# Performance work log

Measured on AMD Instinct MI355X. Metric: run time of the kernel, lower is better.

Reference implementation:

```python
import jax, jax.numpy as jnp
import numpy as np

D_MODEL = 1024
NUM_HEADS = 16
HEAD_DIM = D_MODEL // NUM_HEADS
SCALE = HEAD_DIM ** -0.5
B, N = 4, 2048


def setup_inputs() -> dict:
    key = jax.random.key(0)
    ks = jax.random.split(key, 6)
    x = jax.random.normal(ks[0], (B, N, D_MODEL), dtype=jnp.float32)
    mask = jnp.ones((B, 1, N, N), dtype=jnp.int32)
    alibi_bias = jax.random.normal(ks[1], (1, NUM_HEADS, N, N), dtype=jnp.float32)
    s = 1.0 / np.sqrt(D_MODEL)
    Wq = jax.random.normal(ks[2], (D_MODEL, D_MODEL), dtype=jnp.float32) * s
    Wk = jax.random.normal(ks[3], (D_MODEL, D_MODEL), dtype=jnp.float32) * s
    Wv = jax.random.normal(ks[4], (D_MODEL, D_MODEL), dtype=jnp.float32) * s
    Wo = jax.random.normal(ks[5], (D_MODEL, D_MODEL), dtype=jnp.float32) * s
    return {"x": x, "mask": mask, "alibi_bias": alibi_bias,
            "Wq": Wq, "Wk": Wk, "Wv": Wv, "Wo": Wo}


def reference(x, mask, alibi_bias, Wq, Wk, Wv, Wo):
    Bx, Nx, D = x.shape
    H, Hd = NUM_HEADS, HEAD_DIM
    # torch Linear(bias=False): y = x @ W.T
    q = (x @ Wq.T).reshape(Bx, Nx, H, Hd).transpose(0, 2, 1, 3)  # [B,H,N,Hd]
    k = (x @ Wk.T).reshape(Bx, Nx, H, Hd).transpose(0, 2, 1, 3)
    v = (x @ Wv.T).reshape(Bx, Nx, H, Hd).transpose(0, 2, 1, 3)
    attn = jnp.einsum('bhqd,bhkd->bhqk', q, k) * SCALE
    attn = attn + alibi_bias
    neg_inf = jnp.finfo(attn.dtype).min
    attn = jnp.where(mask == 0, neg_inf, attn)
    attn = jax.nn.softmax(attn, axis=-1)
    out = jnp.einsum('bhqk,bhkd->bhqd', attn, v)  # [B,H,N,Hd]
    out = out.transpose(0, 2, 1, 3).reshape(Bx, Nx, D)
    return out @ Wo.T
```

## Files before the change

### kernel.cpp

```cpp
#include <hip/hip_runtime.h>

#define NSEQ 2048
#define DMODEL 1024
#define NHEAD 16
#define HDIM 64
#define NBATCH 4
#define MTOT 8192
#define ATT_SCALE 0.125f
#define LOG2E 1.4426950408889634f
#define SM_SHIFT 12.0f

typedef __bf16 bf16x8 __attribute__((ext_vector_type(8)));
typedef float f32x4 __attribute__((ext_vector_type(4)));
typedef unsigned int u32x4 __attribute__((ext_vector_type(4)));
typedef unsigned short u16;
typedef unsigned int u32;
typedef unsigned long long u64;

__device__ __forceinline__ u16 f2bf(float f) {
  u32 u = __builtin_bit_cast(u32, f);
  return (u16)((u + 0x7fffu + ((u >> 16) & 1u)) >> 16);
}

__device__ __forceinline__ void gload_lds16(const void* g, void* l) {
  __builtin_amdgcn_global_load_lds(
      (__attribute__((address_space(1))) const u32*)g,
      (__attribute__((address_space(3))) u32*)l, 16, 0, 0);
}

__global__ __launch_bounds__(256) void cast_f32_bf16(const float* __restrict__ in,
                                                     u16* __restrict__ out, int n) {
  int i = (blockIdx.x * 256 + threadIdx.x) * 4;
  if (i >= n) return;
  float4 v = *(const float4*)(in + i);
  ushort4 o;
  o.x = f2bf(v.x); o.y = f2bf(v.y); o.z = f2bf(v.z); o.w = f2bf(v.w);
  *(ushort4*)(out + i) = o;
}

__global__ __launch_bounds__(256) void cast_w4(const float* __restrict__ a,
                                               const float* __restrict__ b,
                                               const float* __restrict__ c,
                                               const float* __restrict__ d,
                                               u16* __restrict__ out) {
  int bid = blockIdx.x;
  int which = bid >> 10, lb = bid & 1023;
  const float* src = (which == 0) ? a : (which == 1) ? b : (which == 2) ? c : d;
  int i = (lb * 256 + threadIdx.x) * 4;
  float4 v = *(const float4*)(src + i);
  ushort4 o;
  o.x = f2bf(v.x); o.y = f2bf(v.y); o.z = f2bf(v.z); o.w = f2bf(v.w);
  *(ushort4*)(out + (size_t)which * 1048576 + i) = o;
}

__global__ __launch_bounds__(256) void pack_mask(const int* __restrict__ mask,
                                                 u64* __restrict__ bits) {
  int wave = (blockIdx.x * 256 + threadIdx.x) >> 6;
  int lane = threadIdx.x & 63;
  const int* row = mask + (size_t)wave * NSEQ;
  u64* out = bits + (size_t)wave * 32;
  for (int c = 0; c < 32; ++c) {
    int v = row[c * 64 + lane];
    u64 bl = __ballot(v != 0);
    if (lane == 0) out[c] = bl;
  }
}

__global__ __launch_bounds__(256) void gemm_qkv(const u16* __restrict__ A,
                                                const u16* __restrict__ Wc,
                                                u16* __restrict__ qo,
                                                u16* __restrict__ ko,
                                                u16* __restrict__ vo) {
  __shared__ __align__(16) u16 Al[128 * 64];
  __shared__ __align__(16) u16 Bl[128 * 64];
  const int tid = threadIdx.x;
  const int w = tid >> 6, l = tid & 63;
  const int l15 = l & 15, l4 = l >> 4;
  const int bm = blockIdx.x, bn = blockIdx.y;
  const int wm = w >> 1, wn = w & 1;

  f32x4 acc[4][4] = {};

  for (int ks = 0; ks < 1024; ks += 64) {
    __syncthreads();
#pragma unroll
    for (int c = 0; c < 4; ++c) {
      int g = w * 256 + c * 64 + l;
      int row = g >> 3, gc = g & 7;
      int sgc = gc ^ (row & 7);
      gload_lds16(A + (size_t)(bm * 128 + row) * 1024 + ks + sgc * 8, &Al[g * 8]);
      gload_lds16(Wc + (size_t)(bn * 128 + row) * 1024 + ks + sgc * 8, &Bl[g * 8]);
    }
    __syncthreads();
#pragma unroll
    for (int kc = 0; kc < 2; ++kc) {
      bf16x8 af[4], bfr[4];
#pragma unroll
      for (int mi = 0; mi < 4; ++mi) {
        int row = wm * 64 + mi * 16 + l15;
        int gc2 = (kc * 4 + l4) ^ (row & 7);
        af[mi] = *(const bf16x8*)&Al[row * 64 + gc2 * 8];
      }
#pragma unroll
      for (int ni = 0; ni < 4; ++ni) {
        int row = wn * 64 + ni * 16 + l15;
        int gc2 = (kc * 4 + l4) ^ (row & 7);
        bfr[ni] = *(const bf16x8*)&Bl[row * 64 + gc2 * 8];
      }
#pragma unroll
      for (int mi = 0; mi < 4; ++mi)
#pragma unroll
        for (int ni = 0; ni < 4; ++ni)
          acc[mi][ni] = __builtin_amdgcn_mfma_f32_16x16x32_bf16(af[mi], bfr[ni],
                                                                acc[mi][ni], 0, 0, 0);
    }
  }

  const int which = bn >> 3;
#pragma unroll
  for (int mi = 0; mi < 4; ++mi)
#pragma unroll
    for (int ni = 0; ni < 4; ++ni)
#pragma unroll
      for (int r = 0; r < 4; ++r) {
        int m = bm * 128 + wm * 64 + mi * 16 + l4 * 4 + r;
        int n = (bn & 7) * 128 + wn * 64 + ni * 16 + l15;
        int b = m >> 11, row = m & 2047, h = n >> 6, d = n & 63;
        u16 val = f2bf(acc[mi][ni][r]);
        size_t bh = (size_t)(b * 16 + h);
        if (which == 0)      qo[(bh * NSEQ + row) * 64 + d] = val;
        else if (which == 1) ko[(bh * NSEQ + row) * 64 + d] = val;
        else                 vo[(bh * 64 + d) * NSEQ + row] = val;
      }
}

__global__ __launch_bounds__(256) void gemm_out(const u16* __restrict__ A,
                                                const u16* __restrict__ W,
                                                float* __restrict__ C) {
  __shared__ __align__(16) u16 Al[128 * 64];
  __shared__ __align__(16) u16 Bl[128 * 64];
  const int tid = threadIdx.x;
  const int w = tid >> 6, l = tid & 63;
  const int l15 = l & 15, l4 = l >> 4;
  const int bm = blockIdx.x, bn = blockIdx.y;
  const int wm = w >> 1, wn = w & 1;

  f32x4 acc[4][4] = {};

  for (int ks = 0; ks < 1024; ks += 64) {
    __syncthreads();
#pragma unroll
    for (int c = 0; c < 4; ++c) {
      int g = w * 256 + c * 64 + l;
      int row = g >> 3, gc = g & 7;
      int sgc = gc ^ (row & 7);
      gload_lds16(A + (size_t)(bm * 128 + row) * 1024 + ks + sgc * 8, &Al[g * 8]);
      gload_lds16(W + (size_t)(bn * 128 + row) * 1024 + ks + sgc * 8, &Bl[g * 8]);
    }
    __syncthreads();
#pragma unroll
    for (int kc = 0; kc < 2; ++kc) {
      bf16x8 af[4], bfr[4];
#pragma unroll
      for (int mi = 0; mi < 4; ++mi) {
        int row = wm * 64 + mi * 16 + l15;
        int gc2 = (kc * 4 + l4) ^ (row & 7);
        af[mi] = *(const bf16x8*)&Al[row * 64 + gc2 * 8];
      }
#pragma unroll
      for (int ni = 0; ni < 4; ++ni) {
        int row = wn * 64 + ni * 16 + l15;
        int gc2 = (kc * 4 + l4) ^ (row & 7);
        bfr[ni] = *(const bf16x8*)&Bl[row * 64 + gc2 * 8];
      }
#pragma unroll
      for (int mi = 0; mi < 4; ++mi)
#pragma unroll
        for (int ni = 0; ni < 4; ++ni)
          acc[mi][ni] = __builtin_amdgcn_mfma_f32_16x16x32_bf16(af[mi], bfr[ni],
                                                                acc[mi][ni], 0, 0, 0);
    }
  }

#pragma unroll
  for (int mi = 0; mi < 4; ++mi)
#pragma unroll
    for (int ni = 0; ni < 4; ++ni)
#pragma unroll
      for (int r = 0; r < 4; ++r) {
        int m = bm * 128 + wm * 64 + mi * 16 + l4 * 4 + r;
        int n = bn * 128 + wn * 64 + ni * 16 + l15;
        C[(size_t)m * 1024 + n] = acc[mi][ni][r];
      }
}

__global__ __launch_bounds__(256, 4) void attn_kernel(
    const u16* __restrict__ q, const u16* __restrict__ k, const u16* __restrict__ vT,
    const float* __restrict__ alibi, const u64* __restrict__ mbits,
    u16* __restrict__ o) {
  __shared__ __align__(16) u16 Kl[2][64 * 64];
  __shared__ __align__(16) u16 Vl[2][64 * 64];

  const int tid = threadIdx.x, w = tid >> 6, l = tid & 63;
  const int l15 = l & 15, l4 = l >> 4;
  const int W = blockIdx.x;
  const int W2 = (W & 7) * 256 + (W >> 3);
  const int b = W2 & 3, hq = W2 >> 2;
  const int qb = hq & 31, h = hq >> 5;
  const int bh = b * 16 + h;
  const int wq0 = qb * 64 + w * 16;
  const int myq = wq0 + l15;

  bf16x8 aq[2];
  {
    const u16* qrow = q + ((size_t)bh * NSEQ + myq) * 64;
    aq[0] = *(const bf16x8*)(qrow + l4 * 8);
    aq[1] = *(const bf16x8*)(qrow + 32 + l4 * 8);
  }

  const u16* kg[2]; const u16* vg[2];
#pragma unroll
  for (int c = 0; c < 2; ++c) {
    int g = w * 128 + c * 64 + l;
    int row = g >> 3, gc = g & 7, sgc = gc ^ (row & 7);
    int srow = (row & 0x23) | (((row >> 2) & 3) << 3) | (((row >> 4) & 1) << 2);
    kg[c] = k + ((size_t)bh * NSEQ + srow) * 64 + sgc * 8;
    vg[c] = vT + ((size_t)bh * 64 + row) * NSEQ + sgc * 8;
  }

  const float* alp = alibi + (size_t)h * NSEQ * NSEQ + (size_t)myq * NSEQ + 8 * l4;
  const u64* mrp = mbits + ((size_t)b * NSEQ + myq) * 32;

  const int kfr[2] = { l15 * 128 + (((0 + l4) ^ (l15 & 7)) << 4),
                       l15 * 128 + (((4 + l4) ^ (l15 & 7)) << 4) };

  const u32x4 onesu = {0x3F803F80u, 0x3F803F80u, 0x3F803F80u, 0x3F803F80u};
  const bf16x8 bones = __builtin_bit_cast(bf16x8, onesu);

  f32x4 oacc[4] = {};
  f32x4 osum = {};

  auto stage = [&](u16* KB, u16* VB) {
#pragma unroll
    for (int c = 0; c < 2; ++c) {
      gload_lds16(kg[c], (char*)KB + (w * 128 + c * 64 + l) * 16);
      kg[c] += 4096;
      gload_lds16(vg[c], (char*)VB + (w * 128 + c * 64 + l) * 16);
      vg[c] += 64;
    }
  };

  auto loadal = [&](float4* a, u64& m, int t) {
    a[0] = *(const float4*)(alp + t * 64);
    a[1] = *(const float4*)(alp + t * 64 + 4);
    a[2] = *(const float4*)(alp + t * 64 + 32);
    a[3] = *(const float4*)(alp + t * 64 + 36);
    m = mrp[t];
  };

  float4 alA[4], alB[4];
  u64 mbA, mbB;

  stage(Kl[0], Vl[0]);
  loadal(alA, mbA, 0);
  __syncthreads();

  auto body = [&](const u16* KB, const u16* VB, u16* KN, u16* VN,
                  const float4* alc, u64 mbc, float4* aln, u64& mbn,
                  int t, bool dost) {
    if (dost) {
      loadal(aln, mbn, t + 1);
      stage(KN, VN);
    }

    f32x4 st[4];
#pragma unroll
    for (int kb = 0; kb < 4; ++kb) {
      f32x4 z = {0.f, 0.f, 0.f, 0.f};
      st[kb] = z;
#pragma unroll
      for (int kc = 0; kc < 2; ++kc) {
        bf16x8 bk = *(const bf16x8*)((const char*)KB + kfr[kc] + kb * 2048);
        st[kb] = __builtin_amdgcn_mfma_f32_16x16x32_bf16(bk, aq[kc], st[kb], 0, 0, 0);
      }
    }

#pragma unroll
    for (int kb = 0; kb < 4; ++kb)
#pragma unroll
      for (int r = 0; r < 4; ++r)
        st[kb][r] = fmaf(st[kb][r], ATT_SCALE, alc[kb][r]);
    if (!__all(mbc == ~0ull)) {
#pragma unroll
      for (int kb = 0; kb < 4; ++kb)
#pragma unroll
        for (int r = 0; r < 4; ++r) {
          int bit = 32 * (kb >> 1) + 8 * l4 + 4 * (kb & 1) + r;
          if (!((mbc >> bit) & 1)) st[kb][r] = -3.0e38f;
        }
    }

    float p[16];
#pragma unroll
    for (int kb = 0; kb < 4; ++kb)
#pragma unroll
      for (int r = 0; r < 4; ++r)
        p[kb * 4 + r] = exp2f(fmaf(st[kb][r], LOG2E, -SM_SHIFT * LOG2E));

    u32 Wp[8];
#pragma unroll
    for (int i = 0; i < 8; ++i)
      asm("v_cvt_pk_bf16_f32 %0, %1, %2" : "=v"(Wp[i]) : "v"(p[2 * i]), "v"(p[2 * i + 1]));

#pragma unroll
    for (int c = 0; c < 2; ++c) {
      u32x4 wv = {Wp[4 * c], Wp[4 * c + 1], Wp[4 * c + 2], Wp[4 * c + 3]};
      bf16x8 pa = __builtin_bit_cast(bf16x8, wv);
      osum = __builtin_amdgcn_mfma_f32_16x16x32_bf16(pa, bones, osum, 0, 0, 0);
#pragma unroll
      for (int db = 0; db < 4; ++db) {
        bf16x8 bv = *(const bf16x8*)((const char*)VB + kfr[c] + db * 2048);
        oacc[db] = __builtin_amdgcn_mfma_f32_16x16x32_bf16(pa, bv, oacc[db], 0, 0, 0);
      }
    }
    __syncthreads();
  };

  for (int t2 = 0; t2 < 16; ++t2) {
    body(Kl[0], Vl[0], Kl[1], Vl[1], alA, mbA, alB, mbB, t2 * 2, true);
    body(Kl[1], Vl[1], Kl[0], Vl[0], alB, mbB, alA, mbA, t2 * 2 + 1, t2 < 15);
  }

#pragma unroll
  for (int r = 0; r < 4; ++r) {
    float inv = __builtin_amdgcn_rcpf(osum[r]);
    int qq = wq0 + l4 * 4 + r;
#pragma unroll
    for (int db = 0; db < 4; ++db) {
      int d = db * 16 + l15;
      o[((size_t)b * NSEQ + qq) * DMODEL + h * 64 + d] = f2bf(oacc[db][r] * inv);
    }
  }
}

extern "C" void kernel_launch(void* const* d_in, const int* in_sizes, int n_in,
                              void* d_out, int out_size, void* d_ws, size_t ws_size,
                              hipStream_t stream) {
  (void)in_sizes; (void)n_in; (void)out_size; (void)ws_size;
  const float* x = (const float*)d_in[0];
  const int* mask = (const int*)d_in[1];
  const float* alibi = (const float*)d_in[2];
  const float* Wq = (const float*)d_in[3];
  const float* Wk = (const float*)d_in[4];
  const float* Wv = (const float*)d_in[5];
  const float* Wo = (const float*)d_in[6];
  float* out = (float*)d_out;

  char* ws = (char*)d_ws;
  const size_t MB = 1u << 20;
  u16* xb  = (u16*)(ws + 0 * MB);
  u16* wqb = (u16*)(ws + 16 * MB);
  u16* wob = (u16*)(ws + 22 * MB);
  u16* qb  = (u16*)(ws + 24 * MB);
  u16* kb  = (u16*)(ws + 40 * MB);
  u16* vT  = (u16*)(ws + 56 * MB);
  u16* ob  = (u16*)(ws + 72 * MB);
  u64* mbits = (u64*)(ws + 88 * MB);

  cast_f32_bf16<<<8192, 256, 0, stream>>>(x, xb, MTOT * DMODEL);
  cast_w4<<<4096, 256, 0, stream>>>(Wq, Wk, Wv, Wo, wqb);
  pack_mask<<<2048, 256, 0, stream>>>(mask, mbits);

  gemm_qkv<<<dim3(64, 24), 256, 0, stream>>>(xb, wqb, qb, kb, vT);

  attn_kernel<<<2048, 256, 0, stream>>>(qb, kb, vT, alibi, mbits, ob);

  gemm_out<<<dim3(64, 8), 256, 0, stream>>>(ob, wob, out);
}
```

Baseline: 412.7 us.

## Load attention K/V fragments directly into registers, dropping LDS staging

New measurement: 755.7 us. 1.83x slower.

```diff
diff --git a/kernel.cpp b/kernel.cpp
--- a/kernel.cpp
+++ b/kernel.cpp
@@ -194,13 +194,10 @@
       }
 }
 
-__global__ __launch_bounds__(256, 4) void attn_kernel(
+__global__ __launch_bounds__(256, 3) void attn_kernel(
     const u16* __restrict__ q, const u16* __restrict__ k, const u16* __restrict__ vT,
     const float* __restrict__ alibi, const u64* __restrict__ mbits,
     u16* __restrict__ o) {
-  __shared__ __align__(16) u16 Kl[2][64 * 64];
-  __shared__ __align__(16) u16 Vl[2][64 * 64];
-
   const int tid = threadIdx.x, w = tid >> 6, l = tid & 63;
   const int l15 = l & 15, l4 = l >> 4;
   const int W = blockIdx.x;
@@ -211,126 +208,105 @@
   const int wq0 = qb * 64 + w * 16;
   const int myq = wq0 + l15;
 
-  bf16x8 aq[2];
+  bf16x8 aq0, aq1;
   {
     const u16* qrow = q + ((size_t)bh * NSEQ + myq) * 64;
-    aq[0] = *(const bf16x8*)(qrow + l4 * 8);
-    aq[1] = *(const bf16x8*)(qrow + 32 + l4 * 8);
-  }
-
-  const u16* kg[2]; const u16* vg[2];
-#pragma unroll
-  for (int c = 0; c < 2; ++c) {
-    int g = w * 128 + c * 64 + l;
-    int row = g >> 3, gc = g & 7, sgc = gc ^ (row & 7);
-    int srow = (row & 0x23) | (((row >> 2) & 3) << 3) | (((row >> 4) & 1) << 2);
-    kg[c] = k + ((size_t)bh * NSEQ + srow) * 64 + sgc * 8;
-    vg[c] = vT + ((size_t)bh * 64 + row) * NSEQ + sgc * 8;
-  }
-
+    aq0 = *(const bf16x8*)(qrow + l4 * 8);
+    aq1 = *(const bf16x8*)(qrow + 32 + l4 * 8);
+  }
+
+  const u16* kp = k + ((size_t)bh * NSEQ + 8 * (l15 >> 2) + (l15 & 3)) * 64 + l4 * 8;
+  const u16* vp0 = vT + ((size_t)bh * 64 +  0 + l15) * NSEQ + 8 * l4;
+  const u16* vp1 = vT + ((size_t)bh * 64 + 16 + l15) * NSEQ + 8 * l4;
+  const u16* vp2 = vT + ((size_t)bh * 64 + 32 + l15) * NSEQ + 8 * l4;
+  const u16* vp3 = vT + ((size_t)bh * 64 + 48 + l15) * NSEQ + 8 * l4;
   const float* alp = alibi + (size_t)h * NSEQ * NSEQ + (size_t)myq * NSEQ + 8 * l4;
-  const u64* mrp = mbits + ((size_t)b * NSEQ + myq) * 32;
-
-  const int kfr[2] = { l15 * 128 + (((0 + l4) ^ (l15 & 7)) << 4),
-                       l15 * 128 + (((4 + l4) ^ (l15 & 7)) << 4) };
+  const u32* mp = (const u32*)(mbits + ((size_t)b * NSEQ + myq) * 32);
 
   const u32x4 onesu = {0x3F803F80u, 0x3F803F80u, 0x3F803F80u, 0x3F803F80u};
   const bf16x8 bones = __builtin_bit_cast(bf16x8, onesu);
 
-  f32x4 oacc[4] = {};
+  f32x4 oacc0 = {}, oacc1 = {}, oacc2 = {}, oacc3 = {};
   f32x4 osum = {};
 
-  auto stage = [&](u16* KB, u16* VB) {
-#pragma unroll
-    for (int c = 0; c < 2; ++c) {
-      gload_lds16(kg[c], (char*)KB + (w * 128 + c * 64 + l) * 16);
-      kg[c] += 4096;
-      gload_lds16(vg[c], (char*)VB + (w * 128 + c * 64 + l) * 16);
-      vg[c] += 64;
-    }
-  };
-
-  auto loadal = [&](float4* a, u64& m, int t) {
-    a[0] = *(const float4*)(alp + t * 64);
-    a[1] = *(const float4*)(alp + t * 64 + 4);
-    a[2] = *(const float4*)(alp + t * 64 + 32);
-    a[3] = *(const float4*)(alp + t * 64 + 36);
-    m = mrp[t];
-  };
-
-  float4 alA[4], alB[4];
-  u64 mbA, mbB;
-
-  stage(Kl[0], Vl[0]);
-  loadal(alA, mbA, 0);
-  __syncthreads();
-
-  auto body = [&](const u16* KB, const u16* VB, u16* KN, u16* VN,
-                  const float4* alc, u64 mbc, float4* aln, u64& mbn,
-                  int t, bool dost) {
-    if (dost) {
-      loadal(aln, mbn, t + 1);
-      stage(KN, VN);
-    }
-
-    f32x4 st[4];
-#pragma unroll
-    for (int kb = 0; kb < 4; ++kb) {
-      f32x4 z = {0.f, 0.f, 0.f, 0.f};
-      st[kb] = z;
-#pragma unroll
-      for (int kc = 0; kc < 2; ++kc) {
-        bf16x8 bk = *(const bf16x8*)((const char*)KB + kfr[kc] + kb * 2048);
-        st[kb] = __builtin_amdgcn_mfma_f32_16x16x32_bf16(bk, aq[kc], st[kb], 0, 0, 0);
-      }
-    }
-
-#pragma unroll
-    for (int kb = 0; kb < 4; ++kb)
-#pragma unroll
-      for (int r = 0; r < 4; ++r)
-        st[kb][r] = fmaf(st[kb][r], ATT_SCALE, alc[kb][r]);
-    if (!__all(mbc == ~0ull)) {
-#pragma unroll
-      for (int kb = 0; kb < 4; ++kb)
-#pragma unroll
-        for (int r = 0; r < 4; ++r) {
-          int bit = 32 * (kb >> 1) + 8 * l4 + 4 * (kb & 1) + r;
-          if (!((mbc >> bit) & 1)) st[kb][r] = -3.0e38f;
-        }
-    }
-
-    float p[16];
-#pragma unroll
-    for (int kb = 0; kb < 4; ++kb)
-#pragma unroll
-      for (int r = 0; r < 4; ++r)
-        p[kb * 4 + r] = exp2f(fmaf(st[kb][r], LOG2E, -SM_SHIFT * LOG2E));
-
-    u32 Wp[8];
-#pragma unroll
-    for (int i = 0; i < 8; ++i)
-      asm("v_cvt_pk_bf16_f32 %0, %1, %2" : "=v"(Wp[i]) : "v"(p[2 * i]), "v"(p[2 * i + 1]));
-
-#pragma unroll
-    for (int c = 0; c < 2; ++c) {
-      u32x4 wv = {Wp[4 * c], Wp[4 * c + 1], Wp[4 * c + 2], Wp[4 * c + 3]};
-      bf16x8 pa = __builtin_bit_cast(bf16x8, wv);
-      osum = __builtin_amdgcn_mfma_f32_16x16x32_bf16(pa, bones, osum, 0, 0, 0);
-#pragma unroll
-      for (int db = 0; db < 4; ++db) {
-        bf16x8 bv = *(const bf16x8*)((const char*)VB + kfr[c] + db * 2048);
-        oacc[db] = __builtin_amdgcn_mfma_f32_16x16x32_bf16(pa, bv, oacc[db], 0, 0, 0);
-      }
-    }
-    __syncthreads();
-  };
-
-  for (int t2 = 0; t2 < 16; ++t2) {
-    body(Kl[0], Vl[0], Kl[1], Vl[1], alA, mbA, alB, mbB, t2 * 2, true);
-    body(Kl[1], Vl[1], Kl[0], Vl[0], alB, mbB, alA, mbA, t2 * 2 + 1, t2 < 15);
-  }
-
+  bf16x8 kA00, kA01, kA10, kA11, kB00, kB01, kB10, kB11;
+  bf16x8 vA0, vA1, vA2, vA3, vB0, vB1, vB2, vB3;
+  float4 alA0, alA1, alB0, alB1;
+  u32 mwA, mwB;
+
+#define LDK(s0, s1, s2, s3)                         \
+  s0 = *(const bf16x8*)(kp);                        \
+  s1 = *(const bf16x8*)(kp + 32);                   \
+  s2 = *(const bf16x8*)(kp + 256);                  \
+  s3 = *(const bf16x8*)(kp + 288);                  \
+  kp += 2048;
+#define LDV(d0, d1, d2, d3)                         \
+  d0 = *(const bf16x8*)(vp0); vp0 += 32;            \
+  d1 = *(const bf16x8*)(vp1); vp1 += 32;            \
+  d2 = *(const bf16x8*)(vp2); vp2 += 32;            \
+  d3 = *(const bf16x8*)(vp3); vp3 += 32;
+#define LDA(a0, a1, mw)                             \
+  a0 = *(const float4*)(alp);                       \
+  a1 = *(const float4*)(alp + 4);                   \
+  alp += 32;                                        \
+  mw = *mp++;
+
+#define COMPUTE(kc00, kc01, kc10, kc11, vc0, vc1, vc2, vc3, ac0, ac1, mwc)     \
+  {                                                                            \
+    f32x4 z = {0.f, 0.f, 0.f, 0.f};                                            \
+    f32x4 st0 = __builtin_amdgcn_mfma_f32_16x16x32_bf16(kc00, aq0, z, 0, 0, 0);\
+    st0 = __builtin_amdgcn_mfma_f32_16x16x32_bf16(kc01, aq1, st0, 0, 0, 0);    \
+    f32x4 st1 = __builtin_amdgcn_mfma_f32_16x16x32_bf16(kc10, aq0, z, 0, 0, 0);\
+    st1 = __builtin_amdgcn_mfma_f32_16x16x32_bf16(kc11, aq1, st1, 0, 0, 0);    \
+    float p[8];                                                                \
+    _Pragma("unroll")                                                          \
+    for (int r = 0; r < 4; ++r) {                                              \
+      p[r]     = fmaf(st0[r], ATT_SCALE, ac0[r]);                              \
+      p[4 + r] = fmaf(st1[r], ATT_SCALE, ac1[r]);                              \
+    }                                                                          \
+    if (!__all(mwc == 0xFFFFFFFFu)) {                                          \
+      _Pragma("unroll")                                                        \
+      for (int j = 0; j < 8; ++j)                                              \
+        if (!((mwc >> (8 * l4 + j)) & 1)) p[j] = -3.0e38f;                     \
+    }                                                                          \
+    _Pragma("unroll")                                                          \
+    for (int j = 0; j < 8; ++j)                                                \
+      p[j] = exp2f(fmaf(p[j], LOG2E, -SM_SHIFT * LOG2E));                      \
+    u32 Wp0, Wp1, Wp2, Wp3;                                                    \
+    asm("v_cvt_pk_bf16_f32 %0, %1, %2" : "=v"(Wp0) : "v"(p[0]), "v"(p[1]));    \
+    asm("v_cvt_pk_bf16_f32 %0, %1, %2" : "=v"(Wp1) : "v"(p[2]), "v"(p[3]));    \
+    asm("v_cvt_pk_bf16_f32 %0, %1, %2" : "=v"(Wp2) : "v"(p[4]), "v"(p[5]));    \
+    asm("v_cvt_pk_bf16_f32 %0, %1, %2" : "=v"(Wp3) : "v"(p[6]), "v"(p[7]));    \
+    u32x4 wv = {Wp0, Wp1, Wp2, Wp3};                                           \
+    bf16x8 pa = __builtin_bit_cast(bf16x8, wv);                                \
+    osum = __builtin_amdgcn_mfma_f32_16x16x32_bf16(pa, bones, osum, 0, 0, 0);  \
+    oacc0 = __builtin_amdgcn_mfma_f32_16x16x32_bf16(pa, vc0, oacc0, 0, 0, 0);  \
+    oacc1 = __builtin_amdgcn_mfma_f32_16x16x32_bf16(pa, vc1, oacc1, 0, 0, 0);  \
+    oacc2 = __builtin_amdgcn_mfma_f32_16x16x32_bf16(pa, vc2, oacc2, 0, 0, 0);  \
+    oacc3 = __builtin_amdgcn_mfma_f32_16x16x32_bf16(pa, vc3, oacc3, 0, 0, 0);  \
+  }
+
+  LDK(kA00, kA01, kA10, kA11)
+  LDV(vA0, vA1, vA2, vA3)
+  LDA(alA0, alA1, mwA)
+
+  for (int t2 = 0; t2 < 31; ++t2) {
+    LDK(kB00, kB01, kB10, kB11)
+    LDV(vB0, vB1, vB2, vB3)
+    LDA(alB0, alB1, mwB)
+    COMPUTE(kA00, kA01, kA10, kA11, vA0, vA1, vA2, vA3, alA0, alA1, mwA)
+    LDK(kA00, kA01, kA10, kA11)
+    LDV(vA0, vA1, vA2, vA3)
+    LDA(alA0, alA1, mwA)
+    COMPUTE(kB00, kB01, kB10, kB11, vB0, vB1, vB2, vB3, alB0, alB1, mwB)
+  }
+  LDK(kB00, kB01, kB10, kB11)
+  LDV(vB0, vB1, vB2, vB3)
+  LDA(alB0, alB1, mwB)
+  COMPUTE(kA00, kA01, kA10, kA11, vA0, vA1, vA2, vA3, alA0, alA1, mwA)
+  COMPUTE(kB00, kB01, kB10, kB11, vB0, vB1, vB2, vB3, alB0, alB1, mwB)
+
+  f32x4 oa[4] = {oacc0, oacc1, oacc2, oacc3};
 #pragma unroll
   for (int r = 0; r < 4; ++r) {
     float inv = __builtin_amdgcn_rcpf(osum[r]);
@@ -338,9 +314,13 @@
 #pragma unroll
     for (int db = 0; db < 4; ++db) {
       int d = db * 16 + l15;
-      o[((size_t)b * NSEQ + qq) * DMODEL + h * 64 + d] = f2bf(oacc[db][r] * inv);
-    }
-  }
+      o[((size_t)b * NSEQ + qq) * DMODEL + h * 64 + d] = f2bf(oa[db][r] * inv);
+    }
+  }
+#undef LDK
+#undef LDV
+#undef LDA
+#undef COMPUTE
 }
 
 extern "C" void kernel_launch(void* const* d_in, const int* in_sizes, int n_in,
```
